# Kernel tuning notes

Measured on AMD Instinct MI355X. Metric: run time of the kernel, lower is better.

## Reference

```python
import jax, jax.numpy as jnp
import numpy as np

KP_THRESHOLD = 20.0
KP_BETA = 0.5
TARGET_ENTROPY = 6.0
LOG2 = 0.6931471805599453

B, C, H, W = 8, 18, 256, 256
N_HYP, K = 1024, 9


def setup_inputs() -> dict:
    key = jax.random.key(0)
    ks = jax.random.split(key, 16)
    inp = {}
    for i, sfx in enumerate(['_L', '_R']):
        o = 8 * i
        inp['vertex_pred' + sfx] = jax.random.normal(ks[o + 0], (B, C, H, W), jnp.float32)
        inp['vertex_gt' + sfx] = jax.random.normal(ks[o + 1], (B, C, H, W), jnp.float32)
        inp['mask' + sfx] = jax.random.randint(ks[o + 2], (B, H, W), 0, 2, jnp.int32)
        inp['seg' + sfx] = jax.random.normal(ks[o + 3], (B, 2, H, W), jnp.float32)
        inp['keypoints' + sfx] = jax.random.normal(ks[o + 4], (B, N_HYP, K, 2), jnp.float32) * 10.0
        inp['scores' + sfx] = jax.random.normal(ks[o + 5], (B, N_HYP, K), jnp.float32)
        inp['kpt_2d' + sfx] = jax.random.normal(ks[o + 6], (B, K, 2), jnp.float32) * 10.0
        inp['offset' + sfx] = jax.random.normal(ks[o + 7], (B, 2), jnp.float32)
    inp['softmax_a'] = jnp.asarray(0.5, jnp.float32)
    inp['epoch'] = 100
    return inp


def _smooth_l1_sum(x, y):
    d = jnp.abs(x - y)
    return jnp.sum(jnp.where(d < 1.0, 0.5 * d * d, d - 0.5))


def _side_losses(vertex_pred, vertex_gt, mask, seg, keypoints, scores, kpt_2d, a):
    w = mask[:, None].astype(jnp.float32)                      # [B,1,H,W]
    vote = _smooth_l1_sum(vertex_pred * w, vertex_gt * w)
    ws = jnp.sum(w)
    vote = jnp.where(ws > 0, vote / jnp.maximum(ws, 1.0) / vertex_gt.shape[1], vote)
    # CrossEntropyLoss (mean over B*H*W pixels)
    logp = jax.nn.log_softmax(seg, axis=1)                     # [B,2,H,W]
    nll = -jnp.take_along_axis(logp, mask[:, None], axis=1)[:, 0]
    seg_loss = jnp.mean(nll)
    # DSAC expected keypoint loss: softmax over hypothesis axis
    probs = jax.nn.softmax(a * scores, axis=1)                 # [B,N,K]
    dist = jnp.linalg.norm(keypoints - kpt_2d[:, None], axis=-1)
    kp_loss = jnp.mean(jnp.sum(probs * dist, axis=1))
    # entropy loss on detached scores (entropy in bits)
    s = jax.lax.stop_gradient(a * scores)
    p = jax.nn.softmax(s, axis=1)
    lp = jax.nn.log_softmax(s, axis=1) / LOG2
    entropy = jnp.mean(-jnp.sum(p * lp, axis=1), axis=1)       # [B]
    ent_loss = jnp.sum(jnp.abs(entropy - TARGET_ENTROPY)) / scores.shape[0]
    return vote, seg_loss, kp_loss, ent_loss


def _epipolar(kp_L, off_L, sc_L, kp_R, off_R, sc_R, a):
    # keypoints detached; add per-image crop offsets -> global coords
    kp_L = jax.lax.stop_gradient(kp_L) + off_L[:, None, None, :]
    kp_R = jax.lax.stop_gradient(kp_R) + off_R[:, None, None, :]
    kL, kR = jax.random.split(jax.random.key(1234))
    idx_L = jax.random.categorical(kL, jax.lax.stop_gradient(a * sc_L), axis=1)  # [B,K]
    idx_R = jax.random.categorical(kR, jax.lax.stop_gradient(a * sc_R), axis=1)
    yL = jnp.take_along_axis(kp_L[..., 1], idx_L[:, None, :], axis=1)[:, 0]      # [B,K]
    yR = jnp.take_along_axis(kp_R[..., 1], idx_R[:, None, :], axis=1)[:, 0]
    d = jnp.abs(yL - yR)  # sqrt((yL-yR)^2)
    d = jnp.where(jnp.isfinite(d), d, 0.0)
    return jnp.mean(d)    # mean over K then over B == global mean


def reference(vertex_pred_L, vertex_gt_L, mask_L, seg_L, keypoints_L, scores_L, kpt_2d_L, offset_L,
              vertex_pred_R, vertex_gt_R, mask_R, seg_R, keypoints_R, scores_R, kpt_2d_R, offset_R,
              softmax_a, epoch):
    vL, sL, kL, eL = _side_losses(vertex_pred_L, vertex_gt_L, mask_L, seg_L, keypoints_L, scores_L, kpt_2d_L, softmax_a)
    vR, sR, kR, eR = _side_losses(vertex_pred_R, vertex_gt_R, mask_R, seg_R, keypoints_R, scores_R, kpt_2d_R, softmax_a)
    vote_loss = (vL + vR) * 0.5
    seg_loss = (sL + sR) * 0.5
    kp_loss = (kL + kR) * 0.5
    entropy_loss = (eL + eR) * 0.5
    kp_w = jax.nn.sigmoid(KP_BETA * (KP_THRESHOLD - jax.lax.stop_gradient(kp_loss)))
    vote_w = 1.0 - kp_w
    if epoch > 49:
        epi = _epipolar(keypoints_L, offset_L, scores_L, keypoints_R, offset_R, scores_R, softmax_a)
        vertex_loss = kp_w * (kp_loss + epi) + vote_w * vote_loss
    else:
        vertex_loss = kp_w * kp_loss + vote_w * vote_loss
    loss = vertex_loss + entropy_loss + seg_loss
    return loss
```

## Files before the change

### kernel.cpp

```cpp
#include <hip/hip_runtime.h>
#include <stdint.h>
#include <math.h>

#define HWPIX 65536
#define NCH   18
#define NHYP  1024
#define NK    9
#define NBK   72
#define INV_LOG2 1.4426950408889634f
#define TINYF 1.1754943508222875e-38f

#define NPIXB 2048
#define NVB_SIDE 1024
#define NSB_SIDE 512

#define OFS_VOTE 64
#define OFS_CNT  (OFS_VOTE + 2 * NVB_SIDE)
#define OFS_SEG  (OFS_CNT  + 2 * NSB_SIDE)
#define OFS_KP   (OFS_SEG  + 2 * NSB_SIDE)
#define OFS_ENT  (OFS_KP   + 2 * NBK)
#define OFS_Y    (OFS_ENT  + 2 * NBK)

typedef float fx4 __attribute__((ext_vector_type(4)));
typedef int   ix4 __attribute__((ext_vector_type(4)));

__host__ __device__ inline void tf2x32(uint32_t k0, uint32_t k1,
                                       uint32_t x0, uint32_t x1,
                                       uint32_t& o0, uint32_t& o1) {
  uint32_t ks2 = k0 ^ k1 ^ 0x1BD11BDAu;
  x0 += k0; x1 += k1;
#define TFR(r) { x0 += x1; x1 = (x1 << (r)) | (x1 >> (32 - (r))); x1 ^= x0; }
  TFR(13) TFR(15) TFR(26) TFR(6)   x0 += k1;  x1 += ks2 + 1u;
  TFR(17) TFR(29) TFR(16) TFR(24)  x0 += ks2; x1 += k0 + 2u;
  TFR(13) TFR(15) TFR(26) TFR(6)   x0 += k0;  x1 += k1 + 3u;
  TFR(17) TFR(29) TFR(16) TFR(24)  x0 += k1;  x1 += ks2 + 4u;
  TFR(13) TFR(15) TFR(26) TFR(6)   x0 += ks2; x1 += k0 + 5u;
#undef TFR
  o0 = x0; o1 = x1;
}

__device__ inline float blk_sum(float v, float* sm) {
  int t = threadIdx.x;
  sm[t] = v; __syncthreads();
  for (int off = 128; off > 0; off >>= 1) {
    if (t < off) sm[t] += sm[t + off];
    __syncthreads();
  }
  float r = sm[0]; __syncthreads();
  return r;
}

__device__ inline float sl1(float x, float y, float w) {
  const float dd = fabsf(x - y) * w;
  return (dd < 1.f) ? 0.5f * dd * dd : dd - 0.5f;
}

__device__ inline float nll2(float s0, float s1, int lbl) {
  const float mx = fmaxf(s0, s1);
  const float mn = fminf(s0, s1);
  const float l = mx + logf(1.0f + expf(mn - mx));
  return l - (lbl ? s1 : s0);
}

__device__ inline fx4 ldnt4(const float* p) {
  return __builtin_nontemporal_load((const fx4*)p);
}
__device__ inline ix4 ldnt4i(const int* p) {
  return __builtin_nontemporal_load((const ix4*)p);
}

__global__ __launch_bounds__(256, 8) void fused_kernel(
    const float* __restrict__ vpL, const float* __restrict__ vgL,
    const int*   __restrict__ mkL, const float* __restrict__ sgL,
    const float* __restrict__ vpR, const float* __restrict__ vgR,
    const int*   __restrict__ mkR, const float* __restrict__ sgR,
    const float* __restrict__ scL, const float* __restrict__ kpL,
    const float* __restrict__ k2L, const float* __restrict__ ofL,
    const float* __restrict__ scR, const float* __restrict__ kpR,
    const float* __restrict__ k2R, const float* __restrict__ ofR,
    const float* __restrict__ aPtr,
    uint32_t kLa, uint32_t kLb, uint32_t kRa, uint32_t kRb,
    float* __restrict__ ws) {
  const int t   = threadIdx.x;
  const int bid = blockIdx.x;

  if (bid < NPIXB) {
    const int side  = bid >> 10;
    const int v     = bid & 1023;
    const int b     = v >> 7;
    const int half  = (v >> 6) & 1;
    const int blk64 = v & 63;
    const int hwq   = blk64 * 256 + t;

    const float* vp = side ? vpR : vpL;
    const float* vg = side ? vgR : vgL;
    const int*   mk = side ? mkR : mkL;
    const float* sg = side ? sgR : sgL;

    const ix4 m4 = ldnt4i(mk + ((size_t)b << 16) + ((size_t)hwq << 2));
    const float w0 = (float)m4.x, w1 = (float)m4.y, w2 = (float)m4.z, w3 = (float)m4.w;

    fx4 s0 = (fx4)0.f, s1 = (fx4)0.f;
    if (half == 0) {
      const size_t soff = ((size_t)b << 17) + ((size_t)hwq << 2);
      s0 = ldnt4(sg + soff);
      s1 = ldnt4(sg + soff + HWPIX);
    }

    const size_t pbase = ((size_t)(b * NCH + half * 9) << 16) + ((size_t)hwq << 2);
    const float* pp = vp + pbase;
    const float* qq = vg + pbase;

    fx4 Pa = ldnt4(pp);              fx4 Qa = ldnt4(qq);
    fx4 Pb = ldnt4(pp + HWPIX);      fx4 Qb = ldnt4(qq + HWPIX);

    float acc = 0.f;
#pragma unroll
    for (int j = 0; j < 9; ++j) {
      fx4 pc, qc;
      if ((j & 1) == 0) {
        pc = Pa; qc = Qa;
        if (j + 2 < 9) { Pa = ldnt4(pp + (size_t)(j + 2) * HWPIX); Qa = ldnt4(qq + (size_t)(j + 2) * HWPIX); }
      } else {
        pc = Pb; qc = Qb;
        if (j + 2 < 9) { Pb = ldnt4(pp + (size_t)(j + 2) * HWPIX); Qb = ldnt4(qq + (size_t)(j + 2) * HWPIX); }
      }
      acc += sl1(pc.x, qc.x, w0);
      acc += sl1(pc.y, qc.y, w1);
      acc += sl1(pc.z, qc.z, w2);
      acc += sl1(pc.w, qc.w, w3);
    }

    __shared__ float smp[256];
    const float rvote = blk_sum(acc, smp);
    if (t == 0) ws[OFS_VOTE + side * NVB_SIDE + v] = rvote;

    if (half == 0) {
      float seg = 0.f;
      seg += nll2(s0.x, s1.x, m4.x);
      seg += nll2(s0.y, s1.y, m4.y);
      seg += nll2(s0.z, s1.z, m4.z);
      seg += nll2(s0.w, s1.w, m4.w);
      const float cnt = w0 + w1 + w2 + w3;
      const float rcnt = blk_sum(cnt, smp);
      const float rseg = blk_sum(seg, smp);
      if (t == 0) {
        const int s = b * 64 + blk64;
        ws[OFS_CNT + side * NSB_SIDE + s] = rcnt;
        ws[OFS_SEG + side * NSB_SIDE + s] = rseg;
      }
    }
    return;
  }

  const int hid  = bid - NPIXB;
  const int side = hid / NBK;
  const int bk   = hid % NBK;
  const float* sc = side ? scR : scL;
  const float* kp = side ? kpR : kpL;
  const float* k2 = side ? k2R : k2L;
  const float* of = side ? ofR : ofL;
  const uint32_t K0 = side ? kRa : kLa;
  const uint32_t K1 = side ? kRb : kLb;
  const int b = bk / NK, k = bk % NK;
  const float a = aPtr[0];
  const float kx = k2[(b * NK + k) * 2 + 0];
  const float ky = k2[(b * NK + k) * 2 + 1];
  const float2* kp2 = (const float2*)kp;

  float s[4], d[4], gv[4];
#pragma unroll
  for (int j = 0; j < 4; ++j) {
    const int n = t + j * 256;
    const size_t idx = ((size_t)b * NHYP + n) * NK + k;
    s[j] = a * sc[idx];
    const float2 xy = kp2[idx];
    const float dx = xy.x - kx, dy = xy.y - ky;
    d[j] = sqrtf(dx * dx + dy * dy);
    uint32_t o0, o1;
    tf2x32(K0, K1, 0u, (uint32_t)idx, o0, o1);
    const uint32_t bits = o0 ^ o1;
    float u = __uint_as_float((bits >> 9) | 0x3F800000u) - 1.0f;
    u = fmaxf(TINYF, u * (1.0f - TINYF) + TINYF);
    gv[j] = -logf(-logf(u)) + s[j];
  }

  __shared__ float sm[256];
  __shared__ int   si[256];

  float mx = fmaxf(fmaxf(s[0], s[1]), fmaxf(s[2], s[3]));
  sm[t] = mx; __syncthreads();
  for (int off = 128; off > 0; off >>= 1) {
    if (t < off) sm[t] = fmaxf(sm[t], sm[t + off]);
    __syncthreads();
  }
  mx = sm[0]; __syncthreads();

  float Z = 0.f, Sd = 0.f, Ss = 0.f;
#pragma unroll
  for (int j = 0; j < 4; ++j) {
    const float e = expf(s[j] - mx);
    Z  += e;
    Sd += e * d[j];
    Ss += e * (s[j] - mx);
  }
  Z  = blk_sum(Z, sm);
  Sd = blk_sum(Sd, sm);
  Ss = blk_sum(Ss, sm);

  float bv = gv[0]; int bi = t;
#pragma unroll
  for (int j = 1; j < 4; ++j) {
    const int n = t + j * 256;
    if (gv[j] > bv) { bv = gv[j]; bi = n; }
  }
  sm[t] = bv; si[t] = bi; __syncthreads();
  for (int off = 128; off > 0; off >>= 1) {
    if (t < off) {
      const float v2 = sm[t + off]; const int i2 = si[t + off];
      if (v2 > sm[t] || (v2 == sm[t] && i2 < si[t])) { sm[t] = v2; si[t] = i2; }
    }
    __syncthreads();
  }

  if (t == 0) {
    ws[OFS_KP  + side * NBK + bk] = Sd / Z;
    ws[OFS_ENT + side * NBK + bk] = (logf(Z) - Ss / Z) * INV_LOG2;
    const int n = si[0];
    ws[OFS_Y + side * NBK + bk] =
        kp2[((size_t)b * NHYP + n) * NK + k].y + of[b * 2 + 1];
  }
}

__global__ __launch_bounds__(256) void final_kernel(
    const int* __restrict__ epochPtr, const float* __restrict__ ws,
    float* __restrict__ out) {
  __shared__ float sm[256];
  const int t = threadIdx.x;
  float voteS[2], cntS[2], segS[2], kpS[2], entS[2];
  for (int side = 0; side < 2; ++side) {
    float a;
    a = 0.f; for (int j = t; j < NVB_SIDE; j += 256) a += ws[OFS_VOTE + side * NVB_SIDE + j];
    voteS[side] = blk_sum(a, sm);
    a = 0.f; for (int j = t; j < NSB_SIDE; j += 256) a += ws[OFS_CNT + side * NSB_SIDE + j];
    cntS[side] = blk_sum(a, sm);
    a = 0.f; for (int j = t; j < NSB_SIDE; j += 256) a += ws[OFS_SEG + side * NSB_SIDE + j];
    segS[side] = blk_sum(a, sm);
    a = (t < NBK) ? ws[OFS_KP + side * NBK + t] : 0.f;
    kpS[side] = blk_sum(a, sm);
    a = 0.f;
    if (t < 8) {
      float es = 0.f;
      for (int k = 0; k < NK; ++k) es += ws[OFS_ENT + side * NBK + t * NK + k];
      a = fabsf(es / (float)NK - 6.0f);
    }
    entS[side] = blk_sum(a, sm);
  }
  float e = 0.f;
  if (t < NBK) {
    const float dy = fabsf(ws[OFS_Y + t] - ws[OFS_Y + NBK + t]);
    e = isfinite(dy) ? dy : 0.f;
  }
  const float epiSum = blk_sum(e, sm);

  if (t == 0) {
    const float voteL = (cntS[0] > 0.f) ? voteS[0] / fmaxf(cntS[0], 1.f) / (float)NCH : voteS[0];
    const float voteR = (cntS[1] > 0.f) ? voteS[1] / fmaxf(cntS[1], 1.f) / (float)NCH : voteS[1];
    const float segL = segS[0] / 524288.f;
    const float segR = segS[1] / 524288.f;
    const float kpLm = kpS[0] / (float)NBK, kpRm = kpS[1] / (float)NBK;
    const float entL = entS[0] / 8.f, entR = entS[1] / 8.f;

    const float vote_loss = 0.5f * (voteL + voteR);
    const float seg_loss  = 0.5f * (segL + segR);
    const float kp_loss   = 0.5f * (kpLm + kpRm);
    const float ent_loss  = 0.5f * (entL + entR);
    const float kp_w  = 1.f / (1.f + expf(-0.5f * (20.f - kp_loss)));
    const float vote_w = 1.f - kp_w;
    float vertex;
    if (epochPtr[0] > 49) {
      const float epi = epiSum / (float)NBK;
      vertex = kp_w * (kp_loss + epi) + vote_w * vote_loss;
    } else {
      vertex = kp_w * kp_loss + vote_w * vote_loss;
    }
    out[0] = vertex + ent_loss + seg_loss;
  }
}

extern "C" void kernel_launch(void* const* d_in, const int* in_sizes, int n_in,
                              void* d_out, int out_size, void* d_ws, size_t ws_size,
                              hipStream_t stream) {
  (void)in_sizes; (void)n_in; (void)out_size; (void)ws_size;
  const float* vpL = (const float*)d_in[0];
  const float* vgL = (const float*)d_in[1];
  const int*   mkL = (const int*)  d_in[2];
  const float* sgL = (const float*)d_in[3];
  const float* kpL = (const float*)d_in[4];
  const float* scL = (const float*)d_in[5];
  const float* k2L = (const float*)d_in[6];
  const float* ofL = (const float*)d_in[7];
  const float* vpR = (const float*)d_in[8];
  const float* vgR = (const float*)d_in[9];
  const int*   mkR = (const int*)  d_in[10];
  const float* sgR = (const float*)d_in[11];
  const float* kpR = (const float*)d_in[12];
  const float* scR = (const float*)d_in[13];
  const float* k2R = (const float*)d_in[14];
  const float* ofR = (const float*)d_in[15];
  const float* aP  = (const float*)d_in[16];
  const int*   epP = (const int*)  d_in[17];
  float* ws  = (float*)d_ws;
  float* out = (float*)d_out;

  uint32_t kLa, kLb, kRa, kRb;
  tf2x32(0u, 1234u, 0u, 0u, kLa, kLb);
  tf2x32(0u, 1234u, 0u, 1u, kRa, kRb);

  fused_kernel<<<NPIXB + 2 * NBK, 256, 0, stream>>>(
      vpL, vgL, mkL, sgL, vpR, vgR, mkR, sgR,
      scL, kpL, k2L, ofL, scR, kpR, k2R, ofR,
      aP, kLa, kLb, kRa, kRb, ws);
  final_kernel<<<1, 256, 0, stream>>>(epP, ws, out);
}
```

Before: 47.56 us.

## Issue all vertex loads upfront and replace LDS tree reductions with wave shuffles

The pixel-block path now issues all 18 nontemporal 16-byte loads through inline asm before waiting once on vmcnt, instead of a two-deep rolling prefetch. This raises memory-level parallelism per wave. The shared-memory tree reductions, with their many __syncthreads, are replaced by 64-lane xor-shuffle wave reductions and a single barrier. The occupancy hint in launch bounds drops from 8 to 4 so the extra registers for the 18 vectors fit, which may lower occupancy.

```diff
diff --git a/kernel.cpp b/kernel.cpp
--- a/kernel.cpp
+++ b/kernel.cpp
@@ -23,6 +23,9 @@
 
 typedef float fx4 __attribute__((ext_vector_type(4)));
 typedef int   ix4 __attribute__((ext_vector_type(4)));
+
+#define GL4NT(dst, ptr) \
+  asm volatile("global_load_dwordx4 %0, %1, off nt" : "=v"(dst) : "v"(ptr) : "memory")
 
 __host__ __device__ inline void tf2x32(uint32_t k0, uint32_t k1,
                                        uint32_t x0, uint32_t x1,
@@ -39,6 +42,12 @@
   o0 = x0; o1 = x1;
 }
 
+__device__ inline float wred(float v) {
+#pragma unroll
+  for (int i = 32; i > 0; i >>= 1) v += __shfl_xor(v, i, 64);
+  return v;
+}
+
 __device__ inline float blk_sum(float v, float* sm) {
   int t = threadIdx.x;
   sm[t] = v; __syncthreads();
@@ -69,7 +78,7 @@
   return __builtin_nontemporal_load((const ix4*)p);
 }
 
-__global__ __launch_bounds__(256, 8) void fused_kernel(
+__global__ __launch_bounds__(256, 4) void fused_kernel(
     const float* __restrict__ vpL, const float* __restrict__ vgL,
     const int*   __restrict__ mkL, const float* __restrict__ sgL,
     const float* __restrict__ vpR, const float* __restrict__ vgR,
@@ -111,43 +120,49 @@
     const float* pp = vp + pbase;
     const float* qq = vg + pbase;
 
-    fx4 Pa = ldnt4(pp);              fx4 Qa = ldnt4(qq);
-    fx4 Pb = ldnt4(pp + HWPIX);      fx4 Qb = ldnt4(qq + HWPIX);
+    fx4 P[9], Q[9];
+#pragma unroll
+    for (int j = 0; j < 9; ++j) {
+      GL4NT(P[j], pp + (size_t)j * HWPIX);
+      GL4NT(Q[j], qq + (size_t)j * HWPIX);
+    }
+    asm volatile("s_waitcnt vmcnt(0)" ::: "memory");
+    __builtin_amdgcn_sched_barrier(0);
 
     float acc = 0.f;
 #pragma unroll
     for (int j = 0; j < 9; ++j) {
-      fx4 pc, qc;
-      if ((j & 1) == 0) {
-        pc = Pa; qc = Qa;
-        if (j + 2 < 9) { Pa = ldnt4(pp + (size_t)(j + 2) * HWPIX); Qa = ldnt4(qq + (size_t)(j + 2) * HWPIX); }
-      } else {
-        pc = Pb; qc = Qb;
-        if (j + 2 < 9) { Pb = ldnt4(pp + (size_t)(j + 2) * HWPIX); Qb = ldnt4(qq + (size_t)(j + 2) * HWPIX); }
-      }
-      acc += sl1(pc.x, qc.x, w0);
-      acc += sl1(pc.y, qc.y, w1);
-      acc += sl1(pc.z, qc.z, w2);
-      acc += sl1(pc.w, qc.w, w3);
-    }
-
-    __shared__ float smp[256];
-    const float rvote = blk_sum(acc, smp);
-    if (t == 0) ws[OFS_VOTE + side * NVB_SIDE + v] = rvote;
-
+      acc += sl1(P[j].x, Q[j].x, w0);
+      acc += sl1(P[j].y, Q[j].y, w1);
+      acc += sl1(P[j].z, Q[j].z, w2);
+      acc += sl1(P[j].w, Q[j].w, w3);
+    }
+
+    __shared__ float smx[12];
+    const int wid = t >> 6, lane = t & 63;
+    const float vw = wred(acc);
+    float cw = 0.f, gw = 0.f;
     if (half == 0) {
+      const float cnt = w0 + w1 + w2 + w3;
       float seg = 0.f;
       seg += nll2(s0.x, s1.x, m4.x);
       seg += nll2(s0.y, s1.y, m4.y);
       seg += nll2(s0.z, s1.z, m4.z);
       seg += nll2(s0.w, s1.w, m4.w);
-      const float cnt = w0 + w1 + w2 + w3;
-      const float rcnt = blk_sum(cnt, smp);
-      const float rseg = blk_sum(seg, smp);
-      if (t == 0) {
+      cw = wred(cnt);
+      gw = wred(seg);
+    }
+    if (lane == 0) {
+      smx[wid] = vw;
+      if (half == 0) { smx[4 + wid] = cw; smx[8 + wid] = gw; }
+    }
+    __syncthreads();
+    if (t == 0) {
+      ws[OFS_VOTE + side * NVB_SIDE + v] = smx[0] + smx[1] + smx[2] + smx[3];
+      if (half == 0) {
         const int s = b * 64 + blk64;
-        ws[OFS_CNT + side * NSB_SIDE + s] = rcnt;
-        ws[OFS_SEG + side * NSB_SIDE + s] = rseg;
+        ws[OFS_CNT + side * NSB_SIDE + s] = smx[4] + smx[5] + smx[6] + smx[7];
+        ws[OFS_SEG + side * NSB_SIDE + s] = smx[8] + smx[9] + smx[10] + smx[11];
       }
     }
     return;
```

Result: slower. 49.45 us (+4.0%).
